# Performance work log

Measured on AMD Instinct MI355X. Metric: run time of the kernel, lower is better.

## Reference

```python
import jax, jax.numpy as jnp
import numpy as np

L, B, T, C, H, V = 8, 8, 1024, 768, 12, 1024
D = C // H  # head dim 64
FF = 4 * C
EPS = 1e-5


def _ln(h, g, b):
    mu = jnp.mean(h, axis=-1, keepdims=True)
    var = jnp.mean((h - mu) ** 2, axis=-1, keepdims=True)
    return (h - mu) * jax.lax.rsqrt(var + EPS) * g + b


def _ffn(h, W1, b1, W2, b2):
    return jax.nn.gelu(h @ W1 + b1, approximate=False) @ W2 + b2


def setup_inputs() -> dict:
    key = jax.random.key(0)
    ks = jax.random.split(key, 16)
    s = 0.02
    inp = {
        "x": jax.random.randint(ks[0], (B, T), 0, V),
        "embed": jax.random.normal(ks[1], (V, C), jnp.float32) * s,
        "pos": jax.random.normal(ks[2], (T, C), jnp.float32) * s,
        "Wqkv": jax.random.normal(ks[3], (L, C, 3 * C), jnp.float32) * s,
        "bqkv": jnp.zeros((L, 3 * C), jnp.float32),
        "W1a": jax.random.normal(ks[4], (L, C, FF), jnp.float32) * s,
        "b1a": jnp.zeros((L, FF), jnp.float32),
        "W2a": jax.random.normal(ks[5], (L, FF, C), jnp.float32) * s,
        "b2a": jnp.zeros((L, C), jnp.float32),
        "g1": jnp.ones((L, C), jnp.float32),
        "beta1": jnp.zeros((L, C), jnp.float32),
        "W1b": jax.random.normal(ks[6], (L, C, FF), jnp.float32) * s,
        "b1b": jnp.zeros((L, FF), jnp.float32),
        "W2b": jax.random.normal(ks[7], (L, FF, C), jnp.float32) * s,
        "b2b": jnp.zeros((L, C), jnp.float32),
        "g2": jnp.ones((L, C), jnp.float32),
        "beta2": jnp.zeros((L, C), jnp.float32),
        "lm_W": jax.random.normal(ks[8], (C, V), jnp.float32) * s,
        "lm_b": jnp.zeros((V,), jnp.float32),
    }
    return inp


def reference(x, embed, pos, Wqkv, bqkv, W1a, b1a, W2a, b2a, g1, beta1,
              W1b, b1b, W2b, b2b, g2, beta2, lm_W, lm_b):
    h = embed[x] + pos[:T]  # (B,T,C)
    causal = jnp.tril(jnp.ones((T, T), bool))

    def block(h, p):
        (Wqkv, bqkv, W1a, b1a, W2a, b2a, g1, beta1,
         W1b, b1b, W2b, b2b, g2, beta2) = p
        qkv = h @ Wqkv + bqkv  # (B,T,3C); split order is K,Q,V per source
        K, Q, Vv = jnp.split(qkv, 3, axis=-1)
        K = K.reshape(B, T, H, D).transpose(0, 2, 1, 3)
        Q = Q.reshape(B, T, H, D).transpose(0, 2, 1, 3)
        Vv = Vv.reshape(B, T, H, D).transpose(0, 2, 1, 3)
        att = jnp.einsum("bhqd,bhkd->bhqk", Q, K) / jnp.sqrt(jnp.float32(D))
        att = jnp.where(causal, att, -jnp.inf)
        att = jax.nn.softmax(att, axis=-1)
        y = jnp.einsum("bhqk,bhkd->bhqd", att, Vv)
        y = y.transpose(0, 2, 1, 3).reshape(B, T, C)
        y = _ffn(y, W1a, b1a, W2a, b2a)  # FFN inside SelfAttn
        h = h + _ln(y, g1, beta1)        # post-norm residual, as in source
        h = h + _ln(_ffn(h, W1b, b1b, W2b, b2b), g2, beta2)
        return h, None

    params = (Wqkv, bqkv, W1a, b1a, W2a, b2a, g1, beta1,
              W1b, b1b, W2b, b2b, g2, beta2)
    h, _ = jax.lax.scan(block, h, params)
    return h @ lm_W + lm_b  # (B,T,V) logits
```

## Files before the change

### kernel.cpp

```cpp
#include <hip/hip_runtime.h>
#include <hip/hip_bf16.h>

#define L_ 8
#define B_ 8
#define T_ 1024
#define C_ 768
#define H_ 12
#define D_HEAD 64
#define V_ 1024
#define FF_ 3072
#define M_ (B_ * T_)

typedef __bf16 bf16x8 __attribute__((ext_vector_type(8)));
typedef float f32x4 __attribute__((ext_vector_type(4)));

typedef const __attribute__((address_space(1))) void* as1cvp;
typedef __attribute__((address_space(3))) void* as3vp;

__device__ __forceinline__ void async16(const void* g, void* l) {
  __builtin_amdgcn_global_load_lds((as1cvp)g, (as3vp)l, 16, 0, 0);
}

__device__ __forceinline__ float bf2f(unsigned short u) {
  union { unsigned u32; float f; } c; c.u32 = ((unsigned)u) << 16; return c.f;
}

__device__ __forceinline__ unsigned short f2bf(float f) {
  __hip_bfloat16 h = __float2bfloat16(f);
  return *(unsigned short*)&h;
}

__device__ __forceinline__ float gelu_f(float x) {
  return 0.5f * x * (1.0f + erff(x * 0.70710678118654752f));
}

__global__ __launch_bounds__(256) void embed_kernel(
    const int* __restrict__ x, const float* __restrict__ emb,
    const float* __restrict__ pos, float* __restrict__ h,
    __hip_bfloat16* __restrict__ hb) {
  int row = blockIdx.x;
  int t = row & (T_ - 1);
  int id = x[row];
#pragma unroll
  for (int j = 0; j < 3; ++j) {
    int c = threadIdx.x + j * 256;
    float v = emb[(size_t)id * C_ + c] + pos[(size_t)t * C_ + c];
    h[(size_t)row * C_ + c] = v;
    hb[(size_t)row * C_ + c] = __float2bfloat16(v);
  }
}

__global__ void transpose_cast(const float* __restrict__ W,
                               __hip_bfloat16* __restrict__ Wt, int K, int N) {
  __shared__ float tile[32][33];
  int nb = blockIdx.x * 32, kb = blockIdx.y * 32;
  int tx = threadIdx.x, ty = threadIdx.y;
#pragma unroll
  for (int r = 0; r < 4; ++r)
    tile[ty + r * 8][tx] = W[(size_t)(kb + ty + r * 8) * N + nb + tx];
  __syncthreads();
#pragma unroll
  for (int r = 0; r < 4; ++r)
    Wt[(size_t)(nb + ty + r * 8) * K + kb + tx] =
        __float2bfloat16(tile[tx][ty + r * 8]);
}

__global__ void transpose_cast2(const float* __restrict__ Wa,
                                __hip_bfloat16* __restrict__ Wta,
                                const float* __restrict__ Wb,
                                __hip_bfloat16* __restrict__ Wtb, int K, int N) {
  __shared__ float tile[32][33];
  const float* W = blockIdx.z ? Wb : Wa;
  __hip_bfloat16* Wt = blockIdx.z ? Wtb : Wta;
  int nb = blockIdx.x * 32, kb = blockIdx.y * 32;
  int tx = threadIdx.x, ty = threadIdx.y;
#pragma unroll
  for (int r = 0; r < 4; ++r)
    tile[ty + r * 8][tx] = W[(size_t)(kb + ty + r * 8) * N + nb + tx];
  __syncthreads();
#pragma unroll
  for (int r = 0; r < 4; ++r)
    Wt[(size_t)(nb + ty + r * 8) * K + kb + tx] =
        __float2bfloat16(tile[tx][ty + r * 8]);
}

template <int ACT_GELU, int OUT_BF16>
__global__ __launch_bounds__(256, 2) void gemm_bt(
    const __hip_bfloat16* __restrict__ A, const __hip_bfloat16* __restrict__ Bt,
    const float* __restrict__ bias, void* __restrict__ Cv, int M, int N, int K) {
  __shared__ __align__(16) __hip_bfloat16 As[128 * 32];
  __shared__ __align__(16) __hip_bfloat16 Bs[128 * 32];
  const int tid = threadIdx.x;
  const int lane = tid & 63, wv = tid >> 6;
  const int lane4 = lane & 15, quad = lane >> 4;
  const int wr = wv >> 1, wc = wv & 1;
  const int bm = blockIdx.y * 128, bn = blockIdx.x * 128;

  const int r0 = tid >> 2, kc0 = (tid & 3) * 8;
  const __hip_bfloat16* gA0 = A + (size_t)(bm + r0) * K + kc0;
  const __hip_bfloat16* gA1 = gA0 + (size_t)64 * K;
  const __hip_bfloat16* gB0 = Bt + (size_t)(bn + r0) * K + kc0;
  const __hip_bfloat16* gB1 = gB0 + (size_t)64 * K;
  __hip_bfloat16* lA0 = As + tid * 8;
  __hip_bfloat16* lA1 = As + (tid + 256) * 8;
  __hip_bfloat16* lB0 = Bs + tid * 8;
  __hip_bfloat16* lB1 = Bs + (tid + 256) * 8;

  f32x4 acc[4][4] = {};

  for (int k0 = 0; k0 < K; k0 += 32) {
    async16(gA0 + k0, lA0);
    async16(gA1 + k0, lA1);
    async16(gB0 + k0, lB0);
    async16(gB1 + k0, lB1);
    __syncthreads();
    bf16x8 af[4], bfv[4];
#pragma unroll
    for (int i = 0; i < 4; ++i)
      af[i] = *(const bf16x8*)(As + (wr * 64 + i * 16 + lane4) * 32 + quad * 8);
#pragma unroll
    for (int j = 0; j < 4; ++j)
      bfv[j] = *(const bf16x8*)(Bs + (wc * 64 + j * 16 + lane4) * 32 + quad * 8);
#pragma unroll
    for (int i = 0; i < 4; ++i)
#pragma unroll
      for (int j = 0; j < 4; ++j)
        acc[i][j] = __builtin_amdgcn_mfma_f32_16x16x32_bf16(af[i], bfv[j],
                                                            acc[i][j], 0, 0, 0);
    __syncthreads();
  }

#pragma unroll
  for (int i = 0; i < 4; ++i) {
    int row0 = bm + wr * 64 + i * 16 + quad * 4;
#pragma unroll
    for (int j = 0; j < 4; ++j) {
      int col = bn + wc * 64 + j * 16 + lane4;
      float bv = bias[col];
#pragma unroll
      for (int r = 0; r < 4; ++r) {
        float v = acc[i][j][r] + bv;
        if (ACT_GELU) v = gelu_f(v);
        size_t off = (size_t)(row0 + r) * N + col;
        if (OUT_BF16)
          ((__hip_bfloat16*)Cv)[off] = __float2bfloat16(v);
        else
          ((float*)Cv)[off] = v;
      }
    }
  }
}

__global__ __launch_bounds__(256) void attn_mfma(
    const __hip_bfloat16* __restrict__ qkv, __hip_bfloat16* __restrict__ y) {
  __shared__ __align__(16) __hip_bfloat16 VtS[64][72];
  __shared__ __align__(16) __hip_bfloat16 Ps[4][16][72];

  const int tid = threadIdx.x;
  const int lane = tid & 63, w = tid >> 6;
  const int lane4 = lane & 15, quad = lane >> 4;
  const int qt = gridDim.x - 1 - blockIdx.x;
  const int bh = blockIdx.y;
  const int b = bh / H_, hh = bh % H_;
  const unsigned short* qk16 = (const unsigned short*)qkv;
  const size_t base = (size_t)b * T_ * (3 * C_) + hh * D_HEAD;

  union FragU { bf16x8 v; unsigned short s[8]; uint4 q; };

  FragU aq[2];
  {
    const unsigned short* qp =
        qk16 + base + (size_t)(qt * 64 + w * 16 + lane4) * (3 * C_) + C_ +
        quad * 8;
#pragma unroll
    for (int c = 0; c < 2; ++c) {
      FragU t;
      t.q = *(const uint4*)(qp + c * 32);
#pragma unroll
      for (int j = 0; j < 8; ++j) aq[c].s[j] = f2bf(bf2f(t.s[j]) * 0.125f);
    }
  }

  const unsigned short* kbase0 =
      qk16 + base + (size_t)(lane4)*(3 * C_) + quad * 8;
  const unsigned short* vbase =
      qk16 + base + (size_t)lane * (3 * C_) + 2 * C_ + w * 16;
  const size_t tile_stride = (size_t)64 * (3 * C_);

  f32x4 o_acc[4] = {};
  float m_r[4] = {-1e30f, -1e30f, -1e30f, -1e30f};
  float l_r[4] = {0.f, 0.f, 0.f, 0.f};

  FragU kc[4][2];
  uint4 vc0, vc1;
  {
    const unsigned short* kp = kbase0;
#pragma unroll
    for (int nt = 0; nt < 4; ++nt) {
      kc[nt][0].q = *(const uint4*)(kp + nt * 16 * (3 * C_));
      kc[nt][1].q = *(const uint4*)(kp + nt * 16 * (3 * C_) + 32);
    }
    vc0 = *(const uint4*)vbase;
    vc1 = *(const uint4*)(vbase + 8);
  }

  for (int kt = 0; kt <= qt; ++kt) {
    FragU kn[4][2];
    uint4 vn0, vn1;
    {
      int ktn = (kt < qt) ? kt + 1 : qt;
      const unsigned short* kp = kbase0 + (size_t)ktn * tile_stride;
#pragma unroll
      for (int nt = 0; nt < 4; ++nt) {
        kn[nt][0].q = *(const uint4*)(kp + nt * 16 * (3 * C_));
        kn[nt][1].q = *(const uint4*)(kp + nt * 16 * (3 * C_) + 32);
      }
      const unsigned short* vp = vbase + (size_t)ktn * tile_stride;
      vn0 = *(const uint4*)vp;
      vn1 = *(const uint4*)(vp + 8);
    }

    f32x4 s_acc[4] = {};
#pragma unroll
    for (int nt = 0; nt < 4; ++nt) {
      s_acc[nt] = __builtin_amdgcn_mfma_f32_16x16x32_bf16(aq[0].v, kc[nt][0].v,
                                                          s_acc[nt], 0, 0, 0);
      s_acc[nt] = __builtin_amdgcn_mfma_f32_16x16x32_bf16(aq[1].v, kc[nt][1].v,
                                                          s_acc[nt], 0, 0, 0);
    }

    if (kt == qt) {
      int qloc = w * 16 + quad * 4;
#pragma unroll
      for (int nt = 0; nt < 4; ++nt) {
        int kloc = nt * 16 + lane4;
#pragma unroll
        for (int r = 0; r < 4; ++r)
          if (kloc > qloc + r) s_acc[nt][r] = -1e30f;
      }
    }

    float p[4][4], alpha[4], ts[4];
#pragma unroll
    for (int r = 0; r < 4; ++r) {
      float tm = fmaxf(fmaxf(s_acc[0][r], s_acc[1][r]),
                       fmaxf(s_acc[2][r], s_acc[3][r]));
      tm = fmaxf(tm, __shfl_xor(tm, 1));
      tm = fmaxf(tm, __shfl_xor(tm, 2));
      tm = fmaxf(tm, __shfl_xor(tm, 4));
      tm = fmaxf(tm, __shfl_xor(tm, 8));
      float mn = fmaxf(m_r[r], tm);
      alpha[r] = __expf(m_r[r] - mn);
      m_r[r] = mn;
      float sr = 0.f;
#pragma unroll
      for (int nt = 0; nt < 4; ++nt) {
        float pv = __expf(s_acc[nt][r] - mn);
        p[nt][r] = pv;
        sr += pv;
      }
      sr += __shfl_xor(sr, 1);
      sr += __shfl_xor(sr, 2);
      sr += __shfl_xor(sr, 4);
      sr += __shfl_xor(sr, 8);
      ts[r] = sr;
    }
#pragma unroll
    for (int r = 0; r < 4; ++r) {
      l_r[r] = l_r[r] * alpha[r] + ts[r];
#pragma unroll
      for (int nt = 0; nt < 4; ++nt) o_acc[nt][r] *= alpha[r];
    }

    __syncthreads();

    {
      const unsigned short* vs = (const unsigned short*)&vc0;
#pragma unroll
      for (int j = 0; j < 8; ++j)
        *(unsigned short*)&VtS[w * 16 + j][lane] = vs[j];
      vs = (const unsigned short*)&vc1;
#pragma unroll
      for (int j = 0; j < 8; ++j)
        *(unsigned short*)&VtS[w * 16 + 8 + j][lane] = vs[j];
    }
#pragma unroll
    for (int nt = 0; nt < 4; ++nt)
#pragma unroll
      for (int r = 0; r < 4; ++r)
        *(unsigned short*)&Ps[w][quad * 4 + r][nt * 16 + lane4] =
            f2bf(p[nt][r]);

    __syncthreads();

    FragU ap0, ap1;
    ap0.v = *(const bf16x8*)&Ps[w][lane4][quad * 8];
    ap1.v = *(const bf16x8*)&Ps[w][lane4][32 + quad * 8];
#pragma unroll
    for (int nt = 0; nt < 4; ++nt) {
      bf16x8 bv0 = *(const bf16x8*)&VtS[nt * 16 + lane4][quad * 8];
      bf16x8 bv1 = *(const bf16x8*)&VtS[nt * 16 + lane4][32 + quad * 8];
      o_acc[nt] = __builtin_amdgcn_mfma_f32_16x16x32_bf16(ap0.v, bv0,
                                                          o_acc[nt], 0, 0, 0);
      o_acc[nt] = __builtin_amdgcn_mfma_f32_16x16x32_bf16(ap1.v, bv1,
                                                          o_acc[nt], 0, 0, 0);
    }

#pragma unroll
    for (int nt = 0; nt < 4; ++nt) {
      kc[nt][0] = kn[nt][0];
      kc[nt][1] = kn[nt][1];
    }
    vc0 = vn0;
    vc1 = vn1;
  }

  float inv[4];
#pragma unroll
  for (int r = 0; r < 4; ++r) inv[r] = 1.f / l_r[r];
#pragma unroll
  for (int nt = 0; nt < 4; ++nt) {
#pragma unroll
    for (int r = 0; r < 4; ++r) {
      int row = qt * 64 + w * 16 + quad * 4 + r;
      __hip_bfloat16* yp =
          y + (size_t)(b * T_ + row) * C_ + hh * D_HEAD + nt * 16 + lane4;
      *yp = __float2bfloat16(o_acc[nt][r] * inv[r]);
    }
  }
}

__global__ __launch_bounds__(256) void resid_ln(
    float* __restrict__ h, const float* __restrict__ z,
    const float* __restrict__ g, const float* __restrict__ be,
    __hip_bfloat16* __restrict__ hb) {
  int row = blockIdx.x;
  int tid = threadIdx.x;
  const float* zr = z + (size_t)row * C_;
  float v[3], s = 0.f, s2 = 0.f;
#pragma unroll
  for (int j = 0; j < 3; ++j) {
    v[j] = zr[tid + 256 * j];
    s += v[j];
    s2 += v[j] * v[j];
  }
#pragma unroll
  for (int msk = 1; msk < 64; msk <<= 1) {
    s += __shfl_xor(s, msk);
    s2 += __shfl_xor(s2, msk);
  }
  __shared__ float red[8];
  int w = tid >> 6;
  if ((tid & 63) == 0) { red[w] = s; red[4 + w] = s2; }
  __syncthreads();
  s = red[0] + red[1] + red[2] + red[3];
  s2 = red[4] + red[5] + red[6] + red[7];
  float mu = s * (1.f / C_);
  float var = s2 * (1.f / C_) - mu * mu;
  float rstd = rsqrtf(var + 1e-5f);
  float* hr = h + (size_t)row * C_;
  __hip_bfloat16* hbr = hb + (size_t)row * C_;
#pragma unroll
  for (int j = 0; j < 3; ++j) {
    int c = tid + 256 * j;
    float nv = hr[c] + (v[j] - mu) * rstd * g[c] + be[c];
    hr[c] = nv;
    hbr[c] = __float2bfloat16(nv);
  }
}

extern "C" void kernel_launch(void* const* d_in, const int* in_sizes, int n_in,
                              void* d_out, int out_size, void* d_ws,
                              size_t ws_size, hipStream_t stream) {
  const int* x = (const int*)d_in[0];
  const float* embed = (const float*)d_in[1];
  const float* pos = (const float*)d_in[2];
  const float* Wqkv = (const float*)d_in[3];
  const float* bqkv = (const float*)d_in[4];
  const float* W1a = (const float*)d_in[5];
  const float* b1a = (const float*)d_in[6];
  const float* W2a = (const float*)d_in[7];
  const float* b2a = (const float*)d_in[8];
  const float* g1 = (const float*)d_in[9];
  const float* be1 = (const float*)d_in[10];
  const float* W1b = (const float*)d_in[11];
  const float* b1b = (const float*)d_in[12];
  const float* W2b = (const float*)d_in[13];
  const float* b2b = (const float*)d_in[14];
  const float* g2 = (const float*)d_in[15];
  const float* be2 = (const float*)d_in[16];
  const float* lmW = (const float*)d_in[17];
  const float* lmb = (const float*)d_in[18];
  float* out = (float*)d_out;

  char* p = (char*)d_ws;
  auto alloc = [&](size_t bytes) {
    void* r = (void*)p;
    p += (bytes + 255) & ~(size_t)255;
    return r;
  };
  float* h = (float*)alloc((size_t)M_ * C_ * 4);
  __hip_bfloat16* hb = (__hip_bfloat16*)alloc((size_t)M_ * C_ * 2);
  __hip_bfloat16* qkv = (__hip_bfloat16*)alloc((size_t)M_ * 3 * C_ * 2);
  __hip_bfloat16* ybuf = (__hip_bfloat16*)alloc((size_t)M_ * C_ * 2);
  __hip_bfloat16* ubuf = (__hip_bfloat16*)alloc((size_t)M_ * FF_ * 2);
  float* zbuf = (float*)alloc((size_t)M_ * C_ * 4);
  __hip_bfloat16* Wtqkv = (__hip_bfloat16*)alloc((size_t)(3 * C_) * C_ * 2);
  __hip_bfloat16* Wt1a = (__hip_bfloat16*)alloc((size_t)FF_ * C_ * 2);
  __hip_bfloat16* Wt1b = (__hip_bfloat16*)alloc((size_t)FF_ * C_ * 2);
  __hip_bfloat16* Wt2a = (__hip_bfloat16*)alloc((size_t)C_ * FF_ * 2);
  __hip_bfloat16* Wt2b = (__hip_bfloat16*)alloc((size_t)C_ * FF_ * 2);

  dim3 blk256(256);
  embed_kernel<<<M_, blk256, 0, stream>>>(x, embed, pos, h, hb);

  for (int l = 0; l < L_; ++l) {
    transpose_cast<<<dim3(3 * C_ / 32, C_ / 32), dim3(32, 8), 0, stream>>>(
        Wqkv + (size_t)l * C_ * 3 * C_, Wtqkv, C_, 3 * C_);
    transpose_cast2<<<dim3(FF_ / 32, C_ / 32, 2), dim3(32, 8), 0, stream>>>(
        W1a + (size_t)l * C_ * FF_, Wt1a, W1b + (size_t)l * C_ * FF_, Wt1b,
        C_, FF_);
    transpose_cast2<<<dim3(C_ / 32, FF_ / 32, 2), dim3(32, 8), 0, stream>>>(
        W2a + (size_t)l * FF_ * C_, Wt2a, W2b + (size_t)l * FF_ * C_, Wt2b,
        FF_, C_);

    gemm_bt<0, 1><<<dim3(3 * C_ / 128, M_ / 128), blk256, 0, stream>>>(
        hb, Wtqkv, bqkv + (size_t)l * 3 * C_, qkv, M_, 3 * C_, C_);
    attn_mfma<<<dim3(T_ / 64, B_ * H_), blk256, 0, stream>>>(qkv, ybuf);
    gemm_bt<1, 1><<<dim3(FF_ / 128, M_ / 128), blk256, 0, stream>>>(
        ybuf, Wt1a, b1a + (size_t)l * FF_, ubuf, M_, FF_, C_);
    gemm_bt<0, 0><<<dim3(C_ / 128, M_ / 128), blk256, 0, stream>>>(
        ubuf, Wt2a, b2a + (size_t)l * C_, zbuf, M_, C_, FF_);
    resid_ln<<<M_, blk256, 0, stream>>>(h, zbuf, g1 + (size_t)l * C_,
                                        be1 + (size_t)l * C_, hb);
    gemm_bt<1, 1><<<dim3(FF_ / 128, M_ / 128), blk256, 0, stream>>>(
        hb, Wt1b, b1b + (size_t)l * FF_, ubuf, M_, FF_, C_);
    gemm_bt<0, 0><<<dim3(C_ / 128, M_ / 128), blk256, 0, stream>>>(
        ubuf, Wt2b, b2b + (size_t)l * C_, zbuf, M_, C_, FF_);
    resid_ln<<<M_, blk256, 0, stream>>>(h, zbuf, g2 + (size_t)l * C_,
                                        be2 + (size_t)l * C_, hb);
  }

  transpose_cast<<<dim3(V_ / 32, C_ / 32), dim3(32, 8), 0, stream>>>(
      lmW, Wtqkv, C_, V_);
  gemm_bt<0, 0><<<dim3(V_ / 128, M_ / 128), blk256, 0, stream>>>(
      hb, Wtqkv, lmb, out, M_, V_, C_);
}
```

Measured before the change: 4.151 ms.

## Pre-transpose V and compute transposed scores to drop attention block syncs

Adds a kernel that writes V transposed per head into a separate buffer, so attention loads V fragments straight from global memory instead of staging them through shared memory. Scores are computed transposed (K as A operand), so each lane holds one query row; the row max and sum need only two cross-quad shuffles, and the two __syncthreads per tile go away because each wave touches only its own P tile. The output is repacked through LDS into 16-byte coalesced stores. In exchange there is an extra kernel launch and an extra read and write of V each layer, plus more registers for the prefetched V fragments.

```diff
diff --git a/kernel.cpp b/kernel.cpp
--- a/kernel.cpp
+++ b/kernel.cpp
@@ -82,6 +82,25 @@
   for (int r = 0; r < 4; ++r)
     Wt[(size_t)(nb + ty + r * 8) * K + kb + tx] =
         __float2bfloat16(tile[tx][ty + r * 8]);
+}
+
+__global__ __launch_bounds__(256) void vtrans_kernel(
+    const __hip_bfloat16* __restrict__ qkv, __hip_bfloat16* __restrict__ vT) {
+  __shared__ __hip_bfloat16 tile[32][33];
+  int bh = blockIdx.z;
+  int b = bh / H_, hh = bh % H_;
+  int t0 = blockIdx.x * 32, d0 = blockIdx.y * 32;
+  int tx = threadIdx.x, ty = threadIdx.y;
+  const __hip_bfloat16* src =
+      qkv + (size_t)b * T_ * (3 * C_) + 2 * C_ + hh * D_HEAD;
+#pragma unroll
+  for (int r = 0; r < 4; ++r)
+    tile[ty + r * 8][tx] = src[(size_t)(t0 + ty + r * 8) * (3 * C_) + d0 + tx];
+  __syncthreads();
+  __hip_bfloat16* dst = vT + (size_t)bh * D_HEAD * T_;
+#pragma unroll
+  for (int r = 0; r < 4; ++r)
+    dst[(size_t)(d0 + ty + r * 8) * T_ + t0 + tx] = tile[tx][ty + r * 8];
 }
 
 template <int ACT_GELU, int OUT_BF16>
@@ -152,8 +171,8 @@
 }
 
 __global__ __launch_bounds__(256) void attn_mfma(
-    const __hip_bfloat16* __restrict__ qkv, __hip_bfloat16* __restrict__ y) {
-  __shared__ __align__(16) __hip_bfloat16 VtS[64][72];
+    const __hip_bfloat16* __restrict__ qkv, const __hip_bfloat16* __restrict__ vT,
+    __hip_bfloat16* __restrict__ y) {
   __shared__ __align__(16) __hip_bfloat16 Ps[4][16][72];
 
   const int tid = threadIdx.x;
@@ -163,6 +182,7 @@
   const int bh = blockIdx.y;
   const int b = bh / H_, hh = bh % H_;
   const unsigned short* qk16 = (const unsigned short*)qkv;
+  const unsigned short* vt16 = (const unsigned short*)vT;
   const size_t base = (size_t)b * T_ * (3 * C_) + hh * D_HEAD;
 
   union FragU { bf16x8 v; unsigned short s[8]; uint4 q; };
@@ -181,128 +201,99 @@
     }
   }
 
-  const unsigned short* kbase0 =
-      qk16 + base + (size_t)(lane4)*(3 * C_) + quad * 8;
+  const unsigned short* kbase = qk16 + base + (size_t)lane4 * (3 * C_) + quad * 8;
   const unsigned short* vbase =
-      qk16 + base + (size_t)lane * (3 * C_) + 2 * C_ + w * 16;
-  const size_t tile_stride = (size_t)64 * (3 * C_);
+      vt16 + ((size_t)bh * D_HEAD + lane4) * T_ + quad * 8;
+  const size_t kstride = (size_t)64 * (3 * C_);
 
   f32x4 o_acc[4] = {};
-  float m_r[4] = {-1e30f, -1e30f, -1e30f, -1e30f};
-  float l_r[4] = {0.f, 0.f, 0.f, 0.f};
-
-  FragU kc[4][2];
-  uint4 vc0, vc1;
-  {
-    const unsigned short* kp = kbase0;
-#pragma unroll
-    for (int nt = 0; nt < 4; ++nt) {
-      kc[nt][0].q = *(const uint4*)(kp + nt * 16 * (3 * C_));
-      kc[nt][1].q = *(const uint4*)(kp + nt * 16 * (3 * C_) + 32);
-    }
-    vc0 = *(const uint4*)vbase;
-    vc1 = *(const uint4*)(vbase + 8);
+  float m = -1e30f, l = 0.f;
+
+  FragU kc[4][2], vc[4][2];
+#pragma unroll
+  for (int nt = 0; nt < 4; ++nt) {
+    kc[nt][0].q = *(const uint4*)(kbase + (size_t)nt * 16 * (3 * C_));
+    kc[nt][1].q = *(const uint4*)(kbase + (size_t)nt * 16 * (3 * C_) + 32);
+    vc[nt][0].q = *(const uint4*)(vbase + (size_t)nt * 16 * T_);
+    vc[nt][1].q = *(const uint4*)(vbase + (size_t)nt * 16 * T_ + 32);
   }
 
   for (int kt = 0; kt <= qt; ++kt) {
-    FragU kn[4][2];
-    uint4 vn0, vn1;
+    FragU kn[4][2], vn[4][2];
     {
       int ktn = (kt < qt) ? kt + 1 : qt;
-      const unsigned short* kp = kbase0 + (size_t)ktn * tile_stride;
+      const unsigned short* kp = kbase + (size_t)ktn * kstride;
+      const unsigned short* vp = vbase + ktn * 64;
 #pragma unroll
       for (int nt = 0; nt < 4; ++nt) {
-        kn[nt][0].q = *(const uint4*)(kp + nt * 16 * (3 * C_));
-        kn[nt][1].q = *(const uint4*)(kp + nt * 16 * (3 * C_) + 32);
+        kn[nt][0].q = *(const uint4*)(kp + (size_t)nt * 16 * (3 * C_));
+        kn[nt][1].q = *(const uint4*)(kp + (size_t)nt * 16 * (3 * C_) + 32);
+        vn[nt][0].q = *(const uint4*)(vp + (size_t)nt * 16 * T_);
+        vn[nt][1].q = *(const uint4*)(vp + (size_t)nt * 16 * T_ + 32);
       }
-      const unsigned short* vp = vbase + (size_t)ktn * tile_stride;
-      vn0 = *(const uint4*)vp;
-      vn1 = *(const uint4*)(vp + 8);
-    }
-
-    f32x4 s_acc[4] = {};
+    }
+
+    f32x4 sT[4] = {};
 #pragma unroll
     for (int nt = 0; nt < 4; ++nt) {
-      s_acc[nt] = __builtin_amdgcn_mfma_f32_16x16x32_bf16(aq[0].v, kc[nt][0].v,
-                                                          s_acc[nt], 0, 0, 0);
-      s_acc[nt] = __builtin_amdgcn_mfma_f32_16x16x32_bf16(aq[1].v, kc[nt][1].v,
-                                                          s_acc[nt], 0, 0, 0);
+      sT[nt] = __builtin_amdgcn_mfma_f32_16x16x32_bf16(kc[nt][0].v, aq[0].v,
+                                                       sT[nt], 0, 0, 0);
+      sT[nt] = __builtin_amdgcn_mfma_f32_16x16x32_bf16(kc[nt][1].v, aq[1].v,
+                                                       sT[nt], 0, 0, 0);
     }
 
     if (kt == qt) {
-      int qloc = w * 16 + quad * 4;
-#pragma unroll
-      for (int nt = 0; nt < 4; ++nt) {
-        int kloc = nt * 16 + lane4;
+      int ql = w * 16 + lane4;
+#pragma unroll
+      for (int nt = 0; nt < 4; ++nt)
 #pragma unroll
         for (int r = 0; r < 4; ++r)
-          if (kloc > qloc + r) s_acc[nt][r] = -1e30f;
+          if (nt * 16 + quad * 4 + r > ql) sT[nt][r] = -1e30f;
+    }
+
+    float tm = sT[0][0];
+#pragma unroll
+    for (int nt = 0; nt < 4; ++nt)
+#pragma unroll
+      for (int r = 0; r < 4; ++r) tm = fmaxf(tm, sT[nt][r]);
+    tm = fmaxf(tm, __shfl_xor(tm, 16));
+    tm = fmaxf(tm, __shfl_xor(tm, 32));
+    float mn = fmaxf(m, tm);
+    float alpha = __expf(m - mn);
+    m = mn;
+    float p[4][4], ts = 0.f;
+#pragma unroll
+    for (int nt = 0; nt < 4; ++nt)
+#pragma unroll
+      for (int r = 0; r < 4; ++r) {
+        float pv = __expf(sT[nt][r] - mn);
+        p[nt][r] = pv;
+        ts += pv;
       }
-    }
-
-    float p[4][4], alpha[4], ts[4];
-#pragma unroll
-    for (int r = 0; r < 4; ++r) {
-      float tm = fmaxf(fmaxf(s_acc[0][r], s_acc[1][r]),
-                       fmaxf(s_acc[2][r], s_acc[3][r]));
-      tm = fmaxf(tm, __shfl_xor(tm, 1));
-      tm = fmaxf(tm, __shfl_xor(tm, 2));
-      tm = fmaxf(tm, __shfl_xor(tm, 4));
-      tm = fmaxf(tm, __shfl_xor(tm, 8));
-      float mn = fmaxf(m_r[r], tm);
-      alpha[r] = __expf(m_r[r] - mn);
-      m_r[r] = mn;
-      float sr = 0.f;
-#pragma unroll
-      for (int nt = 0; nt < 4; ++nt) {
-        float pv = __expf(s_acc[nt][r] - mn);
-        p[nt][r] = pv;
-        sr += pv;
-      }
-      sr += __shfl_xor(sr, 1);
-      sr += __shfl_xor(sr, 2);
-      sr += __shfl_xor(sr, 4);
-      sr += __shfl_xor(sr, 8);
-      ts[r] = sr;
-    }
-#pragma unroll
-    for (int r = 0; r < 4; ++r) {
-      l_r[r] = l_r[r] * alpha[r] + ts[r];
-#pragma unroll
-      for (int nt = 0; nt < 4; ++nt) o_acc[nt][r] *= alpha[r];
-    }
-
-    __syncthreads();
-
-    {
-      const unsigned short* vs = (const unsigned short*)&vc0;
-#pragma unroll
-      for (int j = 0; j < 8; ++j)
-        *(unsigned short*)&VtS[w * 16 + j][lane] = vs[j];
-      vs = (const unsigned short*)&vc1;
-#pragma unroll
-      for (int j = 0; j < 8; ++j)
-        *(unsigned short*)&VtS[w * 16 + 8 + j][lane] = vs[j];
-    }
+    ts += __shfl_xor(ts, 16);
+    ts += __shfl_xor(ts, 32);
+    l = l * alpha + ts;
 #pragma unroll
     for (int nt = 0; nt < 4; ++nt)
 #pragma unroll
-      for (int r = 0; r < 4; ++r)
-        *(unsigned short*)&Ps[w][quad * 4 + r][nt * 16 + lane4] =
-            f2bf(p[nt][r]);
-
-    __syncthreads();
-
+      for (int r = 0; r < 4; ++r) o_acc[nt][r] *= alpha;
+
+#pragma unroll
+    for (int nt = 0; nt < 4; ++nt) {
+      unsigned w01 = (unsigned)f2bf(p[nt][0]) | ((unsigned)f2bf(p[nt][1]) << 16);
+      unsigned w23 = (unsigned)f2bf(p[nt][2]) | ((unsigned)f2bf(p[nt][3]) << 16);
+      *(unsigned*)&Ps[w][lane4][nt * 16 + quad * 4] = w01;
+      *(unsigned*)&Ps[w][lane4][nt * 16 + quad * 4 + 2] = w23;
+    }
     FragU ap0, ap1;
     ap0.v = *(const bf16x8*)&Ps[w][lane4][quad * 8];
     ap1.v = *(const bf16x8*)&Ps[w][lane4][32 + quad * 8];
+
 #pragma unroll
     for (int nt = 0; nt < 4; ++nt) {
-      bf16x8 bv0 = *(const bf16x8*)&VtS[nt * 16 + lane4][quad * 8];
-      bf16x8 bv1 = *(const bf16x8*)&VtS[nt * 16 + lane4][32 + quad * 8];
-      o_acc[nt] = __builtin_amdgcn_mfma_f32_16x16x32_bf16(ap0.v, bv0,
+      o_acc[nt] = __builtin_amdgcn_mfma_f32_16x16x32_bf16(vc[nt][0].v, ap0.v,
                                                           o_acc[nt], 0, 0, 0);
-      o_acc[nt] = __builtin_amdgcn_mfma_f32_16x16x32_bf16(ap1.v, bv1,
+      o_acc[nt] = __builtin_amdgcn_mfma_f32_16x16x32_bf16(vc[nt][1].v, ap1.v,
                                                           o_acc[nt], 0, 0, 0);
     }
 
@@ -310,23 +301,26 @@
     for (int nt = 0; nt < 4; ++nt) {
       kc[nt][0] = kn[nt][0];
       kc[nt][1] = kn[nt][1];
-    }
-    vc0 = vn0;
-    vc1 = vn1;
-  }
-
-  float inv[4];
-#pragma unroll
-  for (int r = 0; r < 4; ++r) inv[r] = 1.f / l_r[r];
-#pragma unroll
-  for (int nt = 0; nt < 4; ++nt) {
-#pragma unroll
-    for (int r = 0; r < 4; ++r) {
-      int row = qt * 64 + w * 16 + quad * 4 + r;
-      __hip_bfloat16* yp =
-          y + (size_t)(b * T_ + row) * C_ + hh * D_HEAD + nt * 16 + lane4;
-      *yp = __float2bfloat16(o_acc[nt][r] * inv[r]);
-    }
+      vc[nt][0] = vn[nt][0];
+      vc[nt][1] = vn[nt][1];
+    }
+  }
+
+  float inv = 1.f / l;
+#pragma unroll
+  for (int nt = 0; nt < 4; ++nt)
+#pragma unroll
+    for (int r = 0; r < 4; ++r)
+      *(unsigned short*)&Ps[w][lane4][nt * 16 + quad * 4 + r] =
+          f2bf(o_acc[nt][r] * inv);
+  {
+    int q = lane & 15, seg = lane >> 4;
+    uint4 p0 = *(const uint4*)&Ps[w][q][seg * 16];
+    uint4 p1 = *(const uint4*)&Ps[w][q][seg * 16 + 8];
+    __hip_bfloat16* yp = y + (size_t)(b * T_ + qt * 64 + w * 16 + q) * C_ +
+                         hh * D_HEAD + seg * 16;
+    *(uint4*)yp = p0;
+    *((uint4*)yp + 1) = p1;
   }
 }
 
@@ -402,6 +396,7 @@
   float* h = (float*)alloc((size_t)M_ * C_ * 4);
   __hip_bfloat16* hb = (__hip_bfloat16*)alloc((size_t)M_ * C_ * 2);
   __hip_bfloat16* qkv = (__hip_bfloat16*)alloc((size_t)M_ * 3 * C_ * 2);
+  __hip_bfloat16* vTb = (__hip_bfloat16*)alloc((size_t)B_ * H_ * D_HEAD * T_ * 2);
   __hip_bfloat16* ybuf = (__hip_bfloat16*)alloc((size_t)M_ * C_ * 2);
   __hip_bfloat16* ubuf = (__hip_bfloat16*)alloc((size_t)M_ * FF_ * 2);
   float* zbuf = (float*)alloc((size_t)M_ * C_ * 4);
@@ -426,7 +421,9 @@
 
     gemm_bt<0, 1><<<dim3(3 * C_ / 128, M_ / 128), blk256, 0, stream>>>(
         hb, Wtqkv, bqkv + (size_t)l * 3 * C_, qkv, M_, 3 * C_, C_);
-    attn_mfma<<<dim3(T_ / 64, B_ * H_), blk256, 0, stream>>>(qkv, ybuf);
+    vtrans_kernel<<<dim3(T_ / 32, D_HEAD / 32, B_ * H_), dim3(32, 8), 0,
+                    stream>>>(qkv, vTb);
+    attn_mfma<<<dim3(T_ / 64, B_ * H_), blk256, 0, stream>>>(qkv, vTb, ybuf);
     gemm_bt<1, 1><<<dim3(FF_ / 128, M_ / 128), blk256, 0, stream>>>(
         ybuf, Wt1a, b1a + (size_t)l * FF_, ubuf, M_, FF_, C_);
     gemm_bt<0, 0><<<dim3(C_ / 128, M_ / 128), blk256, 0, stream>>>(
```

After: 4.605 ms. 10.9% more time.
